# Kernel optimization log

Hardware: AMD Instinct MI355X
Metric: run time of the kernel (lower is better)

## Reference

```python
import jax, jax.numpy as jnp
import numpy as np

N, E = 50000, 800000
IN, HID, HEADS = 64, 32, 4


def setup_inputs() -> dict:
    key = jax.random.key(0)
    ks = jax.random.split(key, 18)
    x = jax.random.normal(ks[0], (N, IN), jnp.float32)
    edge_index = jax.random.randint(ks[1], (2, E), 0, N)

    def lin(k, fan_in, fan_out):
        kw, kb = jax.random.split(k)
        bound = 1.0 / np.sqrt(fan_in)
        W = jax.random.uniform(kw, (fan_in, fan_out), jnp.float32, -bound, bound)
        b = jax.random.uniform(kb, (fan_out,), jnp.float32, -bound, bound)
        return W, b

    # layer 1: in=IN, out=HID per head, heads=HEADS, concat=True -> out dim HID*HEADS
    Wq1, bq1 = lin(ks[2], IN, HEADS * HID)
    Wk1, bk1 = lin(ks[3], IN, HEADS * HID)
    Wv1, bv1 = lin(ks[4], IN, HEADS * HID)
    Ws1, bs1 = lin(ks[5], IN, HEADS * HID)  # root/skip lin
    # layer 2: in=HID*HEADS, out=HID, heads=1, concat=False
    IN2 = HID * HEADS
    Wq2, bq2 = lin(ks[6], IN2, HID)
    Wk2, bk2 = lin(ks[7], IN2, HID)
    Wv2, bv2 = lin(ks[8], IN2, HID)
    Ws2, bs2 = lin(ks[9], IN2, HID)
    return dict(x=x, edge_index=edge_index,
                Wq1=Wq1, bq1=bq1, Wk1=Wk1, bk1=bk1, Wv1=Wv1, bv1=bv1, Ws1=Ws1, bs1=bs1,
                Wq2=Wq2, bq2=bq2, Wk2=Wk2, bk2=bk2, Wv2=Wv2, bv2=bv2, Ws2=Ws2, bs2=bs2)


def transformer_conv(x, src, dst, Wq, bq, Wk, bk, Wv, bv, Ws, bs, heads, out_ch, concat):
    """PyG TransformerConv (eval mode, root_weight=True, beta=False)."""
    n = x.shape[0]
    q = (x @ Wq + bq).reshape(n, heads, out_ch)  # [N,H,C]
    k = (x @ Wk + bk).reshape(n, heads, out_ch)
    v = (x @ Wv + bv).reshape(n, heads, out_ch)
    # per-edge attention logits: q_i . k_j / sqrt(C)
    logits = jnp.einsum('ehc,ehc->eh', q[dst], k[src]) / jnp.sqrt(jnp.float32(out_ch))
    # segment softmax over incoming edges of each target node
    m = jax.ops.segment_max(logits, dst, num_segments=n)          # [N,H]
    p = jnp.exp(logits - m[dst])                                   # [E,H]
    denom = jax.ops.segment_sum(p, dst, num_segments=n)            # [N,H]
    alpha = p / denom[dst]                                         # [E,H]
    agg = jax.ops.segment_sum(alpha[:, :, None] * v[src], dst, num_segments=n)  # [N,H,C]
    if concat:
        o = agg.reshape(n, heads * out_ch)
    else:
        o = agg.mean(axis=1)
    return o + x @ Ws + bs


def reference(x, edge_index,
              Wq1, bq1, Wk1, bk1, Wv1, bv1, Ws1, bs1,
              Wq2, bq2, Wk2, bk2, Wv2, bv2, Ws2, bs2):
    src, dst = edge_index[0], edge_index[1]
    h = transformer_conv(x, src, dst, Wq1, bq1, Wk1, bk1, Wv1, bv1, Ws1, bs1,
                         HEADS, HID, True)
    h = jax.nn.elu(h)
    out = transformer_conv(h, src, dst, Wq2, bq2, Wk2, bk2, Wv2, bv2, Ws2, bs2,
                           1, HID, False)
    return out
```

## Files before the change

### kernel.cpp

```cpp
#include <hip/hip_runtime.h>
#include <hip/hip_bf16.h>
#include <hip/hip_fp8.h>

#define N_NODES 50000
#define N_EDGES 800000
#define HB 3125
#define GB1 1563
#define NBS 49

static constexpr float SCALE = 0.17677669529663687f;

typedef __attribute__((ext_vector_type(8))) short bf16x8;
typedef __attribute__((ext_vector_type(4))) float f32x4;
typedef __attribute__((ext_vector_type(2))) float f32x2;
#define MFMA16 __builtin_amdgcn_mfma_f32_16x16x32_bf16

static __device__ inline unsigned short f2bf(float f) {
    __hip_bfloat16 h = __float2bfloat16(f);
    return __builtin_bit_cast(unsigned short, h);
}
static __device__ inline unsigned char f2fp8(float f) {
    __hip_fp8_e4m3 h(f);
    return __builtin_bit_cast(unsigned char, h);
}
static __device__ inline float2 bfpair(unsigned u) {
    return make_float2(__uint_as_float(u << 16),
                       __uint_as_float(u & 0xffff0000u));
}
static __device__ inline float dot8f8(const float* q, uint2 u) {
    f32x2 a = __builtin_amdgcn_cvt_pk_f32_fp8(u.x, false);
    f32x2 b = __builtin_amdgcn_cvt_pk_f32_fp8(u.x, true);
    f32x2 c = __builtin_amdgcn_cvt_pk_f32_fp8(u.y, false);
    f32x2 d = __builtin_amdgcn_cvt_pk_f32_fp8(u.y, true);
    return q[0]*a[0] + q[1]*a[1] + q[2]*b[0] + q[3]*b[1]
         + q[4]*c[0] + q[5]*c[1] + q[6]*d[0] + q[7]*d[1];
}
static __device__ inline float dot8(const float* q, uint4 u) {
    float2 a = bfpair(u.x), b = bfpair(u.y), c = bfpair(u.z), d = bfpair(u.w);
    return q[0]*a.x + q[1]*a.y + q[2]*b.x + q[3]*b.y
         + q[4]*c.x + q[5]*c.y + q[6]*d.x + q[7]*d.y;
}
static __device__ inline void acc8(float* acc, float w, uint4 u) {
    float2 a = bfpair(u.x), b = bfpair(u.y), c = bfpair(u.z), d = bfpair(u.w);
    acc[0] += w*a.x; acc[1] += w*a.y; acc[2] += w*b.x; acc[3] += w*b.y;
    acc[4] += w*c.x; acc[5] += w*c.y; acc[6] += w*d.x; acc[7] += w*d.y;
}
static __device__ inline void unpack8(float* o, uint4 u) {
    float2 a = bfpair(u.x), b = bfpair(u.y), c = bfpair(u.z), d = bfpair(u.w);
    o[0]=a.x; o[1]=a.y; o[2]=b.x; o[3]=b.y; o[4]=c.x; o[5]=c.y; o[6]=d.x; o[7]=d.y;
}
static __device__ inline bf16x8 cvt8(const float* p) {
    float4 f0 = *(const float4*)p;
    float4 f1 = *(const float4*)(p + 4);
    bf16x8 r;
    r[0] = (short)f2bf(f0.x); r[1] = (short)f2bf(f0.y);
    r[2] = (short)f2bf(f0.z); r[3] = (short)f2bf(f0.w);
    r[4] = (short)f2bf(f1.x); r[5] = (short)f2bf(f1.y);
    r[6] = (short)f2bf(f1.z); r[7] = (short)f2bf(f1.w);
    return r;
}


__global__ __launch_bounds__(256) void k_heads(
    const int* __restrict__ dst, int* __restrict__ cnt, int* __restrict__ rank,
    const float* __restrict__ Wq1, const float* __restrict__ Wk1,
    const float* __restrict__ Wv1, const float* __restrict__ Ws1,
    const float* __restrict__ Wq2, const float* __restrict__ Wk2,
    const float* __restrict__ Wv2, const float* __restrict__ Ws2,
    unsigned short* __restrict__ Wf1, unsigned short* __restrict__ Wf2)
{
    if (blockIdx.x < HB) {
        int e = blockIdx.x * 256 + threadIdx.x;
        rank[e] = atomicAdd(&cnt[dst[e]], 1);
        return;
    }
    int id = (blockIdx.x - HB) * 256 + threadIdx.x;
    if (id < 32768) {
        int j = id & 7, l = (id >> 3) & 63, ks = (id >> 9) & 1, nt = (id >> 10) & 7, m = (id >> 13) & 3;
        const float* W = (m == 0) ? Wq1 : (m == 1) ? Wk1 : (m == 2) ? Wv1 : Ws1;
        int k = ks * 32 + ((l >> 4) << 3) + j;
        int c = nt * 16 + (l & 15);
        Wf1[id] = f2bf(W[k * 128 + c]);
    } else if (id < 49152) {
        int id2 = id - 32768;
        int j = id2 & 7, l = (id2 >> 3) & 63, ks = (id2 >> 9) & 3, g = (id2 >> 11) & 7;
        int m = g >> 1, t = g & 1;
        const float* W = (m == 0) ? Wq2 : (m == 1) ? Wk2 : (m == 2) ? Wv2 : Ws2;
        int k = ks * 32 + ((l >> 4) << 3) + j;
        int c = t * 16 + (l & 15);
        Wf2[id2] = f2bf(W[k * 32 + c]);
    }
}


__global__ __launch_bounds__(256) void k_scan(const int* __restrict__ cnt,
                                              int* __restrict__ row,
                                              int* __restrict__ bsum,
                                              int* __restrict__ boff,
                                              int* __restrict__ ctr, int n) {
    __shared__ int wsum[4];
    __shared__ int lastBlk;
    int t = threadIdx.x;
    int base = blockIdx.x * 1024 + t * 4;
    int v0 = (base + 0 < n) ? cnt[base + 0] : 0;
    int v1 = (base + 1 < n) ? cnt[base + 1] : 0;
    int v2 = (base + 2 < n) ? cnt[base + 2] : 0;
    int v3 = (base + 3 < n) ? cnt[base + 3] : 0;
    int s = v0 + v1 + v2 + v3;
    int lane = t & 63, wid = t >> 6;
    int sc = s;
#pragma unroll
    for (int d = 1; d < 64; d <<= 1) {
        int o = __shfl_up(sc, d);
        if (lane >= d) sc += o;
    }
    if (lane == 63) wsum[wid] = sc;
    __syncthreads();
    int woff = 0;
    for (int w = 0; w < wid; ++w) woff += wsum[w];
    int excl = woff + sc - s;
    if (base + 0 < n) row[base + 0] = excl;
    if (base + 1 < n) row[base + 1] = excl + v0;
    if (base + 2 < n) row[base + 2] = excl + v0 + v1;
    if (base + 3 < n) row[base + 3] = excl + v0 + v1 + v2;
    if (t == 255) {
        bsum[blockIdx.x] = woff + sc;
        __threadfence();
        lastBlk = (atomicAdd(ctr, 1) == (int)gridDim.x - 1);
    }
    __syncthreads();
    if (lastBlk && t < 64) {
        __threadfence();
        int v = (t < NBS) ? ((volatile int*)bsum)[t] : 0;
        int sc2 = v;
#pragma unroll
        for (int d = 1; d < 64; d <<= 1) {
            int o = __shfl_up(sc2, d);
            if (t >= d) sc2 += o;
        }
        boff[t] = sc2 - v;
        if (t == (N_NODES >> 10)) row[N_NODES] = N_EDGES - (sc2 - v);
    }
}


__global__ __launch_bounds__(256) void k_work(
    const int* __restrict__ src, const int* __restrict__ dst,
    const int* __restrict__ row, const int* __restrict__ boff,
    const int* __restrict__ rank, int* __restrict__ col,
    const float* __restrict__ x, const unsigned short* __restrict__ Wf1,
    const float* __restrict__ bq, const float* __restrict__ bk,
    const float* __restrict__ bv, const float* __restrict__ bs,
    unsigned short* __restrict__ qs1, unsigned char* __restrict__ k8,
    unsigned short* __restrict__ v1, int n)
{
    if (blockIdx.x < HB) {
        int e = blockIdx.x * 256 + threadIdx.x;
        int de = dst[e];
        col[row[de] + boff[de >> 10] + rank[e]] = src[e];
        return;
    }
    int w = threadIdx.x >> 6;
    int l = threadIdx.x & 63;
    int rb = (blockIdx.x - HB) * 32;
    int lr = l & 15, lk = l >> 4;
    f32x4 acc[2][8];
#pragma unroll
    for (int mt = 0; mt < 2; ++mt)
#pragma unroll
        for (int nt = 0; nt < 8; ++nt) acc[mt][nt] = (f32x4){0.f, 0.f, 0.f, 0.f};
#pragma unroll
    for (int ks = 0; ks < 2; ++ks) {
        bf16x8 a[2];
#pragma unroll
        for (int mt = 0; mt < 2; ++mt) {
            int r = rb + mt * 16 + lr;
            if (r >= n) r = n - 1;
            a[mt] = cvt8(x + (size_t)r * 64 + ks * 32 + lk * 8);
        }
#pragma unroll
        for (int nt = 0; nt < 8; ++nt) {
            bf16x8 b = *(const bf16x8*)(Wf1 + (size_t)((w * 8 + nt) * 1024 + ks * 512 + l * 8));
            acc[0][nt] = MFMA16(a[0], b, acc[0][nt], 0, 0, 0);
            acc[1][nt] = MFMA16(a[1], b, acc[1][nt], 0, 0, 0);
        }
    }
    const float* bptr = (w == 0) ? bq : (w == 1) ? bk : (w == 2) ? bv : bs;
    if (w == 1) {
#pragma unroll
        for (int nt = 0; nt < 8; ++nt) {
            int c = nt * 16 + lr;
            float bias = bptr[c];
#pragma unroll
            for (int mt = 0; mt < 2; ++mt)
#pragma unroll
                for (int i = 0; i < 4; ++i) {
                    int r = rb + mt * 16 + lk * 4 + i;
                    if (r < n) k8[(size_t)r * 128 + c] = f2fp8(acc[mt][nt][i] + bias);
                }
        }
    } else {
        unsigned short* outp = (w == 0) ? qs1 : (w == 3) ? qs1 + 128 : v1;
        size_t stride = (w == 2) ? 128 : 256;
#pragma unroll
        for (int nt = 0; nt < 8; ++nt) {
            int c = nt * 16 + lr;
            float bias = bptr[c];
#pragma unroll
            for (int mt = 0; mt < 2; ++mt)
#pragma unroll
                for (int i = 0; i < 4; ++i) {
                    int r = rb + mt * 16 + lk * 4 + i;
                    if (r < n) outp[(size_t)r * stride + c] = f2bf(acc[mt][nt][i] + bias);
                }
        }
    }
}


__global__ __launch_bounds__(256) void k_gemm2m(
    const unsigned short* __restrict__ h1b, const unsigned short* __restrict__ Wf2,
    const float* __restrict__ bq, const float* __restrict__ bk,
    const float* __restrict__ bv, const float* __restrict__ bs,
    unsigned short* __restrict__ qs2, unsigned short* __restrict__ kv2, int n)
{
    int w = threadIdx.x >> 6;
    int l = threadIdx.x & 63;
    int half = w & 1;
    int rb = blockIdx.x * 64 + (w >> 1) * 32;
    int lr = l & 15, lk = l >> 4;
    f32x4 acc[2][4];
#pragma unroll
    for (int mt = 0; mt < 2; ++mt)
#pragma unroll
        for (int nt = 0; nt < 4; ++nt) acc[mt][nt] = (f32x4){0.f, 0.f, 0.f, 0.f};
#pragma unroll
    for (int ks = 0; ks < 4; ++ks) {
        bf16x8 a[2];
#pragma unroll
        for (int mt = 0; mt < 2; ++mt) {
            int r = rb + mt * 16 + lr;
            if (r >= n) r = n - 1;
            a[mt] = *(const bf16x8*)(h1b + (size_t)r * 128 + ks * 32 + lk * 8);
        }
#pragma unroll
        for (int nt = 0; nt < 4; ++nt) {
            int g = half * 4 + nt;
            bf16x8 b = *(const bf16x8*)(Wf2 + (size_t)((g * 4 + ks) * 512 + l * 8));
            acc[0][nt] = MFMA16(a[0], b, acc[0][nt], 0, 0, 0);
            acc[1][nt] = MFMA16(a[1], b, acc[1][nt], 0, 0, 0);
        }
    }
#pragma unroll
    for (int nt = 0; nt < 4; ++nt) {
        int g = half * 4 + nt;
        int mat = g >> 1;
        int c = (g * 16 + lr) & 31;
        const float* bp = (mat == 0) ? bq : (mat == 1) ? bk : (mat == 2) ? bv : bs;
        unsigned short* outp = (mat == 0) ? qs2 : (mat == 3) ? qs2 + 32
                             : (mat == 1) ? kv2 : kv2 + 32;
        float bias = bp[c];
#pragma unroll
        for (int mt = 0; mt < 2; ++mt) {
#pragma unroll
            for (int i = 0; i < 4; ++i) {
                int r = rb + mt * 16 + lk * 4 + i;
                if (r < n)
                    outp[(size_t)r * 64 + c] = f2bf(acc[mt][nt][i] + bias);
            }
        }
    }
}


__global__ __launch_bounds__(256) void k_agg1(
    const unsigned short* __restrict__ qs1, const unsigned char* __restrict__ k8,
    const unsigned short* __restrict__ v1,
    const int* __restrict__ row, const int* __restrict__ boff,
    const int* __restrict__ col, uint4* __restrict__ h1b, int n)
{
    int i = blockIdx.x * 4 + (threadIdx.x >> 6);
    if (i >= n) return;
    int lane = threadIdx.x & 63;
    int slot = lane >> 4, w = lane & 15;
    float q[8];
    unpack8(q, *(const uint4*)(qs1 + (size_t)i * 256 + w * 8));
    float acc[8] = {};
    float d = 0.f;
    int s = row[i] + boff[i >> 10];
    int e = row[i + 1] + boff[(i + 1) >> 10];
    for (int t = s; t < e; t += 8) {
        int ta = t + slot, tb = t + 4 + slot;
        bool va = ta < e, vb = tb < e;
        int ja = col[va ? ta : s];
        int jb = col[vb ? tb : s];
        uint2 ka = *(const uint2*)(k8 + (size_t)ja * 128 + w * 8);
        uint2 kb = *(const uint2*)(k8 + (size_t)jb * 128 + w * 8);
        uint4 vA = *(const uint4*)(v1 + (size_t)ja * 128 + w * 8);
        uint4 vB = *(const uint4*)(v1 + (size_t)jb * 128 + w * 8);
        float la = dot8f8(q, ka);
        float lb = dot8f8(q, kb);
        la += __shfl_xor(la, 1);  lb += __shfl_xor(lb, 1);
        la += __shfl_xor(la, 2);  lb += __shfl_xor(lb, 2);
        float wa = va ? __expf(la * SCALE) : 0.f;
        float wb = vb ? __expf(lb * SCALE) : 0.f;
        d += wa + wb;
        acc8(acc, wa, vA);
        acc8(acc, wb, vB);
    }
#pragma unroll
    for (int m = 16; m <= 32; m <<= 1) {
        d += __shfl_xor(d, m);
#pragma unroll
        for (int c = 0; c < 8; ++c) acc[c] += __shfl_xor(acc[c], m);
    }
    if (slot == 0) {
        float inv = (d > 0.f) ? 1.f / d : 0.f;
        float sv[8];
        unpack8(sv, *(const uint4*)(qs1 + (size_t)i * 256 + 128 + w * 8));
        unsigned o[4];
#pragma unroll
        for (int p = 0; p < 4; ++p) {
            float rx = acc[2 * p] * inv + sv[2 * p];
            float ry = acc[2 * p + 1] * inv + sv[2 * p + 1];
            rx = (rx > 0.f) ? rx : expm1f(rx);
            ry = (ry > 0.f) ? ry : expm1f(ry);
            o[p] = ((unsigned)f2bf(ry) << 16) | (unsigned)f2bf(rx);
        }
        h1b[(size_t)i * 16 + w] = make_uint4(o[0], o[1], o[2], o[3]);
    }
}


__global__ __launch_bounds__(256) void k_agg2(
    const unsigned short* __restrict__ qs2, const unsigned short* __restrict__ kv2,
    const int* __restrict__ row, const int* __restrict__ boff,
    const int* __restrict__ col, float* __restrict__ out, int n)
{
    int i = blockIdx.x * 4 + (threadIdx.x >> 6);
    if (i >= n) return;
    int lane = threadIdx.x & 63;
    int slot = lane >> 2, qr = lane & 3;
    float q[8];
    unpack8(q, *(const uint4*)(qs2 + (size_t)i * 64 + qr * 8));
    float acc[8] = {};
    float d = 0.f;
    int s = row[i] + boff[i >> 10];
    int e = row[i + 1] + boff[(i + 1) >> 10];
    for (int t = s; t < e; t += 16) {
        int te = t + slot;
        bool va = te < e;
        int j = col[va ? te : s];
        const unsigned short* p = kv2 + (size_t)j * 64;
        uint4 ku = *(const uint4*)(p + qr * 8);
        uint4 vu = *(const uint4*)(p + 32 + qr * 8);
        float lg = dot8(q, ku);
        lg += __shfl_xor(lg, 1);
        lg += __shfl_xor(lg, 2);
        float wv = va ? __expf(lg * SCALE) : 0.f;
        d += wv;
        acc8(acc, wv, vu);
    }
#pragma unroll
    for (int m = 4; m <= 32; m <<= 1) {
        d += __shfl_xor(d, m);
#pragma unroll
        for (int c = 0; c < 8; ++c) acc[c] += __shfl_xor(acc[c], m);
    }
    if (slot == 0) {
        float inv = (d > 0.f) ? 1.f / d : 0.f;
        float sv[8];
        unpack8(sv, *(const uint4*)(qs2 + (size_t)i * 64 + 32 + qr * 8));
        float4 o0, o1;
        o0.x = acc[0] * inv + sv[0];
        o0.y = acc[1] * inv + sv[1];
        o0.z = acc[2] * inv + sv[2];
        o0.w = acc[3] * inv + sv[3];
        o1.x = acc[4] * inv + sv[4];
        o1.y = acc[5] * inv + sv[5];
        o1.z = acc[6] * inv + sv[6];
        o1.w = acc[7] * inv + sv[7];
        *(float4*)&out[(size_t)i * 32 + qr * 8] = o0;
        *(float4*)&out[(size_t)i * 32 + qr * 8 + 4] = o1;
    }
}


extern "C" void kernel_launch(void* const* d_in, const int* in_sizes, int n_in,
                              void* d_out, int out_size, void* d_ws, size_t ws_size,
                              hipStream_t stream)
{
    const int N = N_NODES, E = N_EDGES;
    const float* x   = (const float*)d_in[0];
    const int* edge  = (const int*)d_in[1];
    const int* src   = edge;
    const int* dst   = edge + E;
    const float* Wq1 = (const float*)d_in[2];  const float* bq1 = (const float*)d_in[3];
    const float* Wk1 = (const float*)d_in[4];  const float* bk1 = (const float*)d_in[5];
    const float* Wv1 = (const float*)d_in[6];  const float* bv1 = (const float*)d_in[7];
    const float* Ws1 = (const float*)d_in[8];  const float* bs1 = (const float*)d_in[9];
    const float* Wq2 = (const float*)d_in[10]; const float* bq2 = (const float*)d_in[11];
    const float* Wk2 = (const float*)d_in[12]; const float* bk2 = (const float*)d_in[13];
    const float* Wv2 = (const float*)d_in[14]; const float* bv2 = (const float*)d_in[15];
    const float* Ws2 = (const float*)d_in[16]; const float* bs2 = (const float*)d_in[17];

    char* ws = (char*)d_ws;
    size_t off = 0;
    auto alloc = [&](size_t bytes) -> void* {
        void* p = ws + off;
        off += (bytes + 255) & ~(size_t)255;
        return p;
    };
    unsigned short* qs1 = (unsigned short*)alloc((size_t)N * 256 * 2);
    unsigned char*  k8  = (unsigned char*)alloc((size_t)N * 128);
    unsigned short* v1  = (unsigned short*)alloc((size_t)N * 128 * 2);
    unsigned short* h1b = (unsigned short*)alloc((size_t)N * 128 * 2);
    unsigned short* qs2 = (unsigned short*)alloc((size_t)N * 64 * 2);
    unsigned short* kv2 = (unsigned short*)alloc((size_t)N * 64 * 2);
    unsigned short* Wf1 = (unsigned short*)alloc(32768 * 2);
    unsigned short* Wf2 = (unsigned short*)alloc(16384 * 2);
    int* row_ptr  = (int*)alloc((size_t)(N + 1) * 4);
    int* cnt      = (int*)alloc((size_t)(N + 64) * 4);
    int* ctr      = cnt + N;
    int* rank     = (int*)alloc((size_t)E * 4);
    int* colb     = (int*)alloc((size_t)E * 4);
    int* bsum     = (int*)alloc(64 * 4);
    int* boff     = (int*)alloc(64 * 4);

    hipMemsetAsync(cnt, 0, (size_t)(N + 64) * 4, stream);
    k_heads<<<HB + 192, 256, 0, stream>>>(dst, cnt, rank,
                                          Wq1, Wk1, Wv1, Ws1, Wq2, Wk2, Wv2, Ws2,
                                          Wf1, Wf2);
    k_scan<<<NBS, 256, 0, stream>>>(cnt, row_ptr, bsum, boff, ctr, N);
    k_work<<<HB + GB1, 256, 0, stream>>>(src, dst, row_ptr, boff, rank, colb,
                                         x, Wf1, bq1, bk1, bv1, bs1, qs1, k8, v1, N);
    k_agg1<<<(N + 3) / 4, 256, 0, stream>>>(qs1, k8, v1, row_ptr, boff, colb, (uint4*)h1b, N);
    k_gemm2m<<<(N + 63) / 64, 256, 0, stream>>>(h1b, Wf2, bq2, bk2, bv2, bs2, qs2, kv2, N);
    k_agg2<<<(N + 3) / 4, 256, 0, stream>>>(qs2, kv2, row_ptr, boff, colb, (float*)d_out, N);
}
```

Baseline: 183.5 us.

## Regroup kernels and stage GEMM epilogues through LDS for vectorized stores

```diff
diff --git a/kernel.cpp b/kernel.cpp
--- a/kernel.cpp
+++ b/kernel.cpp
@@ -61,20 +61,14 @@
 }
 
 
-__global__ __launch_bounds__(256) void k_heads(
-    const int* __restrict__ dst, int* __restrict__ cnt, int* __restrict__ rank,
+__global__ __launch_bounds__(256) void k_prep(
     const float* __restrict__ Wq1, const float* __restrict__ Wk1,
     const float* __restrict__ Wv1, const float* __restrict__ Ws1,
     const float* __restrict__ Wq2, const float* __restrict__ Wk2,
     const float* __restrict__ Wv2, const float* __restrict__ Ws2,
     unsigned short* __restrict__ Wf1, unsigned short* __restrict__ Wf2)
 {
-    if (blockIdx.x < HB) {
-        int e = blockIdx.x * 256 + threadIdx.x;
-        rank[e] = atomicAdd(&cnt[dst[e]], 1);
-        return;
-    }
-    int id = (blockIdx.x - HB) * 256 + threadIdx.x;
+    int id = blockIdx.x * 256 + threadIdx.x;
     if (id < 32768) {
         int j = id & 7, l = (id >> 3) & 63, ks = (id >> 9) & 1, nt = (id >> 10) & 7, m = (id >> 13) & 3;
         const float* W = (m == 0) ? Wq1 : (m == 1) ? Wk1 : (m == 2) ? Wv1 : Ws1;
@@ -89,6 +83,93 @@
         int k = ks * 32 + ((l >> 4) << 3) + j;
         int c = t * 16 + (l & 15);
         Wf2[id2] = f2bf(W[k * 32 + c]);
+    }
+}
+
+
+__global__ __launch_bounds__(256) void k_big(
+    const int* __restrict__ dst, int* __restrict__ cnt, int* __restrict__ rank,
+    const float* __restrict__ x, const unsigned short* __restrict__ Wf1,
+    const float* __restrict__ bq, const float* __restrict__ bk,
+    const float* __restrict__ bv, const float* __restrict__ bs,
+    unsigned short* __restrict__ qs1, unsigned char* __restrict__ k8,
+    unsigned short* __restrict__ v1, int n)
+{
+    __shared__ unsigned char smem[4 * 8704];
+    if (blockIdx.x >= GB1) {
+        int e = (blockIdx.x - GB1) * 256 + threadIdx.x;
+        rank[e] = atomicAdd(&cnt[dst[e]], 1);
+        return;
+    }
+    int w = threadIdx.x >> 6;
+    int l = threadIdx.x & 63;
+    int rb = blockIdx.x * 32;
+    int lr = l & 15, lk = l >> 4;
+    f32x4 acc[2][8];
+#pragma unroll
+    for (int mt = 0; mt < 2; ++mt)
+#pragma unroll
+        for (int nt = 0; nt < 8; ++nt) acc[mt][nt] = (f32x4){0.f, 0.f, 0.f, 0.f};
+#pragma unroll
+    for (int ks = 0; ks < 2; ++ks) {
+        bf16x8 a[2];
+#pragma unroll
+        for (int mt = 0; mt < 2; ++mt) {
+            int r = rb + mt * 16 + lr;
+            if (r >= n) r = n - 1;
+            a[mt] = cvt8(x + (size_t)r * 64 + ks * 32 + lk * 8);
+        }
+#pragma unroll
+        for (int nt = 0; nt < 8; ++nt) {
+            bf16x8 b = *(const bf16x8*)(Wf1 + (size_t)((w * 8 + nt) * 1024 + ks * 512 + l * 8));
+            acc[0][nt] = MFMA16(a[0], b, acc[0][nt], 0, 0, 0);
+            acc[1][nt] = MFMA16(a[1], b, acc[1][nt], 0, 0, 0);
+        }
+    }
+    const float* bptr = (w == 0) ? bq : (w == 1) ? bk : (w == 2) ? bv : bs;
+    unsigned char* my = smem + w * 8704;
+    if (w == 1) {
+        unsigned char* lb = my;
+#pragma unroll
+        for (int nt = 0; nt < 8; ++nt) {
+            float bias = bptr[nt * 16 + lr];
+#pragma unroll
+            for (int mt = 0; mt < 2; ++mt)
+#pragma unroll
+                for (int i = 0; i < 4; ++i)
+                    lb[(mt * 16 + lk * 4 + i) * 144 + nt * 16 + lr] = f2fp8(acc[mt][nt][i] + bias);
+        }
+#pragma unroll
+        for (int p = 0; p < 8; ++p) {
+            int rl = p * 4 + lk;
+            int r = rb + rl;
+            if (r < n) {
+                uint2 val = *(const uint2*)(lb + rl * 144 + lr * 8);
+                *(uint2*)(k8 + (size_t)r * 128 + lr * 8) = val;
+            }
+        }
+    } else {
+        unsigned short* ls = (unsigned short*)my;
+#pragma unroll
+        for (int nt = 0; nt < 8; ++nt) {
+            float bias = bptr[nt * 16 + lr];
+#pragma unroll
+            for (int mt = 0; mt < 2; ++mt)
+#pragma unroll
+                for (int i = 0; i < 4; ++i)
+                    ls[(mt * 16 + lk * 4 + i) * 136 + nt * 16 + lr] = f2bf(acc[mt][nt][i] + bias);
+        }
+        unsigned short* outp = (w == 0) ? qs1 : (w == 3) ? qs1 + 128 : v1;
+        size_t stride = (w == 2) ? 128 : 256;
+#pragma unroll
+        for (int p = 0; p < 8; ++p) {
+            int rl = p * 4 + lk;
+            int r = rb + rl;
+            if (r < n) {
+                uint4 val = *(const uint4*)(ls + rl * 136 + lr * 8);
+                *(uint4*)(outp + (size_t)r * stride + lr * 8) = val;
+            }
+        }
     }
 }
 
@@ -144,77 +225,12 @@
 }
 
 
-__global__ __launch_bounds__(256) void k_work(
-    const int* __restrict__ src, const int* __restrict__ dst,
-    const int* __restrict__ row, const int* __restrict__ boff,
-    const int* __restrict__ rank, int* __restrict__ col,
-    const float* __restrict__ x, const unsigned short* __restrict__ Wf1,
-    const float* __restrict__ bq, const float* __restrict__ bk,
-    const float* __restrict__ bv, const float* __restrict__ bs,
-    unsigned short* __restrict__ qs1, unsigned char* __restrict__ k8,
-    unsigned short* __restrict__ v1, int n)
-{
-    if (blockIdx.x < HB) {
-        int e = blockIdx.x * 256 + threadIdx.x;
-        int de = dst[e];
-        col[row[de] + boff[de >> 10] + rank[e]] = src[e];
-        return;
-    }
-    int w = threadIdx.x >> 6;
-    int l = threadIdx.x & 63;
-    int rb = (blockIdx.x - HB) * 32;
-    int lr = l & 15, lk = l >> 4;
-    f32x4 acc[2][8];
-#pragma unroll
-    for (int mt = 0; mt < 2; ++mt)
-#pragma unroll
-        for (int nt = 0; nt < 8; ++nt) acc[mt][nt] = (f32x4){0.f, 0.f, 0.f, 0.f};
-#pragma unroll
-    for (int ks = 0; ks < 2; ++ks) {
-        bf16x8 a[2];
-#pragma unroll
-        for (int mt = 0; mt < 2; ++mt) {
-            int r = rb + mt * 16 + lr;
-            if (r >= n) r = n - 1;
-            a[mt] = cvt8(x + (size_t)r * 64 + ks * 32 + lk * 8);
-        }
-#pragma unroll
-        for (int nt = 0; nt < 8; ++nt) {
-            bf16x8 b = *(const bf16x8*)(Wf1 + (size_t)((w * 8 + nt) * 1024 + ks * 512 + l * 8));
-            acc[0][nt] = MFMA16(a[0], b, acc[0][nt], 0, 0, 0);
-            acc[1][nt] = MFMA16(a[1], b, acc[1][nt], 0, 0, 0);
-        }
-    }
-    const float* bptr = (w == 0) ? bq : (w == 1) ? bk : (w == 2) ? bv : bs;
-    if (w == 1) {
-#pragma unroll
-        for (int nt = 0; nt < 8; ++nt) {
-            int c = nt * 16 + lr;
-            float bias = bptr[c];
-#pragma unroll
-            for (int mt = 0; mt < 2; ++mt)
-#pragma unroll
-                for (int i = 0; i < 4; ++i) {
-                    int r = rb + mt * 16 + lk * 4 + i;
-                    if (r < n) k8[(size_t)r * 128 + c] = f2fp8(acc[mt][nt][i] + bias);
-                }
-        }
-    } else {
-        unsigned short* outp = (w == 0) ? qs1 : (w == 3) ? qs1 + 128 : v1;
-        size_t stride = (w == 2) ? 128 : 256;
-#pragma unroll
-        for (int nt = 0; nt < 8; ++nt) {
-            int c = nt * 16 + lr;
-            float bias = bptr[c];
-#pragma unroll
-            for (int mt = 0; mt < 2; ++mt)
-#pragma unroll
-                for (int i = 0; i < 4; ++i) {
-                    int r = rb + mt * 16 + lk * 4 + i;
-                    if (r < n) outp[(size_t)r * stride + c] = f2bf(acc[mt][nt][i] + bias);
-                }
-        }
-    }
+__global__ void k_scat(const int* __restrict__ src, const int* __restrict__ dst,
+                       const int* __restrict__ row, const int* __restrict__ boff,
+                       const int* __restrict__ rank, int* __restrict__ col) {
+    int e = blockIdx.x * 256 + threadIdx.x;
+    int de = dst[e];
+    col[row[de] + boff[de >> 10] + rank[e]] = src[e];
 }
 
 
@@ -224,6 +240,7 @@
     const float* __restrict__ bv, const float* __restrict__ bs,
     unsigned short* __restrict__ qs2, unsigned short* __restrict__ kv2, int n)
 {
+    __shared__ unsigned short lds[4][32][72];
     int w = threadIdx.x >> 6;
     int l = threadIdx.x & 63;
     int half = w & 1;
@@ -257,17 +274,25 @@
         int mat = g >> 1;
         int c = (g * 16 + lr) & 31;
         const float* bp = (mat == 0) ? bq : (mat == 1) ? bk : (mat == 2) ? bv : bs;
-        unsigned short* outp = (mat == 0) ? qs2 : (mat == 3) ? qs2 + 32
-                             : (mat == 1) ? kv2 : kv2 + 32;
         float bias = bp[c];
 #pragma unroll
-        for (int mt = 0; mt < 2; ++mt) {
-#pragma unroll
-            for (int i = 0; i < 4; ++i) {
-                int r = rb + mt * 16 + lk * 4 + i;
-                if (r < n)
-                    outp[(size_t)r * 64 + c] = f2bf(acc[mt][nt][i] + bias);
-            }
+        for (int mt = 0; mt < 2; ++mt)
+#pragma unroll
+            for (int i = 0; i < 4; ++i)
+                lds[w][mt * 16 + lk * 4 + i][nt * 16 + lr] = f2bf(acc[mt][nt][i] + bias);
+    }
+    unsigned short* outA = (half == 0) ? qs2 : kv2 + 32;
+    unsigned short* outB = (half == 0) ? kv2 : qs2 + 32;
+    int rl8 = l >> 3, ci = (l & 7) * 4;
+#pragma unroll
+    for (int p = 0; p < 4; ++p) {
+        int rl = p * 8 + rl8;
+        int r = rb + rl;
+        if (r < n) {
+            uint2 va = *(const uint2*)&lds[w][rl][ci];
+            *(uint2*)(outA + (size_t)r * 64 + ci) = va;
+            uint2 vb = *(const uint2*)&lds[w][rl][32 + ci];
+            *(uint2*)(outB + (size_t)r * 64 + ci) = vb;
         }
     }
 }
@@ -428,12 +453,11 @@
     int* boff     = (int*)alloc(64 * 4);
 
     hipMemsetAsync(cnt, 0, (size_t)(N + 64) * 4, stream);
-    k_heads<<<HB + 192, 256, 0, stream>>>(dst, cnt, rank,
-                                          Wq1, Wk1, Wv1, Ws1, Wq2, Wk2, Wv2, Ws2,
-                                          Wf1, Wf2);
+    k_prep<<<192, 256, 0, stream>>>(Wq1, Wk1, Wv1, Ws1, Wq2, Wk2, Wv2, Ws2, Wf1, Wf2);
+    k_big<<<GB1 + HB, 256, 0, stream>>>(dst, cnt, rank,
+                                        x, Wf1, bq1, bk1, bv1, bs1, qs1, k8, v1, N);
     k_scan<<<NBS, 256, 0, stream>>>(cnt, row_ptr, bsum, boff, ctr, N);
-    k_work<<<HB + GB1, 256, 0, stream>>>(src, dst, row_ptr, boff, rank, colb,
-                                         x, Wf1, bq1, bk1, bv1, bs1, qs1, k8, v1, N);
+    k_scat<<<HB, 256, 0, stream>>>(src, dst, row_ptr, boff, rank, colb);
     k_agg1<<<(N + 3) / 4, 256, 0, stream>>>(qs1, k8, v1, row_ptr, boff, colb, (uint4*)h1b, N);
     k_gemm2m<<<(N + 63) / 64, 256, 0, stream>>>(h1b, Wf2, bq2, bk2, bv2, bs2, qs2, kv2, N);
     k_agg2<<<(N + 3) / 4, 256, 0, stream>>>(qs2, kv2, row_ptr, boff, colb, (float*)d_out, N);
```

New measurement: 162.7 us. -11.3%, faster.
